# Kernel optimization log

Measured on AMD Instinct MI355X. Metric: run time of the kernel, lower is better.

Reference implementation:

```python
import jax, jax.numpy as jnp
import numpy as np


def setup_inputs() -> dict:
    key = jax.random.key(0)
    k1, k2, k3, k4, k5 = jax.random.split(key, 5)
    B, F, E, NF = 16384, 1024, 64, 32
    return {
        "input": jax.random.normal(k1, (B, F), dtype=jnp.float32),
        "fields": jax.random.randint(k2, (F,), 0, NF, dtype=jnp.int32),
        "w_weight": jax.random.normal(k3, (1, F), dtype=jnp.float32) * 0.02,
        "w_bias": jax.random.normal(k4, (1,), dtype=jnp.float32) * 0.02,
        "vs": jax.random.normal(k5, (NF, F, E), dtype=jnp.float32) * 0.05,
    }


def reference(input, fields, w_weight, w_bias, vs):
    # Linear (1st-order) term: [B, 1]
    linear = input @ w_weight.T + w_bias

    F = input.shape[1]
    # Gather field-aware embedding tables per feature: G[k, i, e] = vs[fields[k], i, e]
    G = vs[fields]  # [F, F, E]
    # A[i, j] = dot(vs[fields[j], i, :], vs[fields[i], j, :])
    A = jnp.einsum("jie,ije->ij", G, G)  # [F, F]
    # P[i, j] = sum_b input[b, i] * input[b, j]  (original sums over batch)
    P = input.T @ input  # [F, F]
    # second_order = sum_{i < j} A[i, j] * P[i, j]  (scalar, as in the source)
    second_order = jnp.sum(jnp.triu(A * P, k=1))

    return jax.nn.sigmoid(linear + second_order)
```

## Files before the change

### kernel.cpp

```cpp
#include <hip/hip_runtime.h>
#include <hip/hip_fp16.h>
#include <math.h>
#include <stdint.h>

#define FDIM 1024
#define BTOT 16384
#define EDIM 64
#define NFLD 32
#define NPANEL 4
#define NPAIRS 10

typedef _Float16 half8 __attribute__((ext_vector_type(8)));
typedef __fp16 fp16x2 __attribute__((ext_vector_type(2)));
typedef float f32x4 __attribute__((ext_vector_type(4)));

__device__ __forceinline__ uint32_t pk2(float a, float b){
  fp16x2 h = __builtin_amdgcn_cvt_pkrtz(a, b);
  return __builtin_bit_cast(uint32_t, h);
}

__device__ __forceinline__ void gload16(const void* g, void* l){
  __builtin_amdgcn_global_load_lds((const __attribute__((address_space(1))) void*)g,
                                   (__attribute__((address_space(3))) void*)l,
                                   16, 0, 0);
}

__device__ __forceinline__ float fget(const float4& v, int i){
  switch (i){ case 0: return v.x; case 1: return v.y; case 2: return v.z; default: return v.w; }
}

__device__ __forceinline__ int pairId(int ti, int tj){
  return ti * NPANEL - (ti * (ti + 1)) / 2 + tj;
}

__device__ __forceinline__ int CMAP(int col){
  return ((col & 3) << 6) | ((col >> 2) ^ ((col & 3) << 1));
}

__global__ __launch_bounds__(256) void transpose_kernel(
    const float* __restrict__ X, const float* __restrict__ w,
    uint4* __restrict__ Xbt, float* __restrict__ linp){
  const int t = threadIdx.x;
  const int bx = blockIdx.x;
  const int p  = bx & 3;
  const int kb = bx >> 2;
  const int ro = t >> 6;
  const int l  = t & 63;
  const int og = kb * 4 + ro;
  const int k0 = og * 8;
  const int c0 = p * 256;

  const float4 w4 = *(const float4*)(w + c0 + 4 * l);

  float4 rv[8];
#pragma unroll
  for (int r = 0; r < 8; ++r)
    rv[r] = *(const float4*)(X + (size_t)(k0 + r) * FDIM + c0 + 4 * l);

  uint4* dst = Xbt + ((size_t)p * 2048 + og) * 256;
#pragma unroll
  for (int i = 0; i < 4; ++i){
    uint4 ch;
    ch.x = pk2(fget(rv[0], i), fget(rv[1], i));
    ch.y = pk2(fget(rv[2], i), fget(rv[3], i));
    ch.z = pk2(fget(rv[4], i), fget(rv[5], i));
    ch.w = pk2(fget(rv[6], i), fget(rv[7], i));
    dst[(i << 6) | (l ^ (i << 1))] = ch;
  }

#pragma unroll
  for (int r = 0; r < 8; ++r){
    float lp = rv[r].x * w4.x + rv[r].y * w4.y + rv[r].z * w4.z + rv[r].w * w4.w;
#pragma unroll
    for (int off = 32; off; off >>= 1) lp += __shfl_xor(lp, off, 64);
    if (l == 0) linp[(size_t)p * BTOT + k0 + r] = lp;
  }
}

__global__ __launch_bounds__(256) void w2_kernel(
    const float* __restrict__ vs, const int* __restrict__ fields,
    _Float16* __restrict__ Wp){
  __shared__ float Si[32][68];
  __shared__ float Sj[32][68];
  __shared__ int gI[32], gJ[32];
  __shared__ int cnt[NFLD], pos[NFLD], off[NFLD + 1];
  __shared__ int permS[FDIM];
  const int t = threadIdx.x;

  if (t < NFLD) cnt[t] = 0;
  __syncthreads();
#pragma unroll
  for (int r = 0; r < 4; ++r) atomicAdd(&cnt[fields[t + 256 * r]], 1);
  __syncthreads();
  if (t == 0){
    int s = 0;
    for (int i = 0; i < NFLD; ++i){ off[i] = s; s += cnt[i]; }
    off[NFLD] = s;
  }
  __syncthreads();
  if (t < NFLD) pos[t] = off[t];
  __syncthreads();
#pragma unroll
  for (int r = 0; r < 4; ++r){
    const int idx = t + 256 * r;
    const int p = atomicAdd(&pos[fields[idx]], 1);
    permS[p] = idx;
  }
  __syncthreads();

  const int a = blockIdx.x >> 5, b = blockIdx.x & 31;
  const int oa = off[a], na = off[a + 1] - oa;
  const int ob = off[b], nb_ = off[b + 1] - ob;
  if (na == 0 || nb_ == 0) return;
  for (int ia0 = 0; ia0 < na; ia0 += 32){
    const int nac = min(32, na - ia0);
    for (int jb0 = 0; jb0 < nb_; jb0 += 32){
      const int nbc = min(32, nb_ - jb0);
      __syncthreads();
      if (t < 32){
        gI[t] = (t < nac) ? permS[oa + ia0 + t] : 0;
        gJ[t] = (t < nbc) ? permS[ob + jb0 + t] : 0;
      }
      __syncthreads();
#pragma unroll
      for (int rep = 0; rep < 2; ++rep){
        const int lidx = rep * 256 + t;
        const int r = lidx >> 4, e4 = (lidx & 15) * 4;
        if (r < nac)
          *(float4*)&Si[r][e4] = *(const float4*)(vs + ((size_t)b * FDIM + gI[r]) * EDIM + e4);
        if (r < nbc)
          *(float4*)&Sj[r][e4] = *(const float4*)(vs + ((size_t)a * FDIM + gJ[r]) * EDIM + e4);
      }
      __syncthreads();
      const int jr = t & 31;
      const int ir0 = t >> 5;
      for (int ko = 0; ko * 8 < nac; ++ko){
        const int ir = ko * 8 + ir0;
        if (ir < nac && jr < nbc){
          float dot = 0.f;
#pragma unroll
          for (int e4 = 0; e4 < EDIM; e4 += 4){
            const float4 x = *(const float4*)&Si[ir][e4];
            const float4 y = *(const float4*)&Sj[jr][e4];
            dot += x.x * y.x + x.y * y.y + x.z * y.z + x.w * y.w;
          }
          const int gi = gI[ir], gj = gJ[jr];
          const int pi = gi >> 8, pj = gj >> 8;
          if (pi <= pj){
            const float v = (gj > gi) ? dot : 0.f;
            const int li = gi & 255, lj = gj & 255;
            const int P  = pairId(pi, pj);
            const int w8 = (li >> 7) * 4 + (lj >> 6);
            const int mb = (li >> 4) & 7, r_ = li & 3;
            const int lane = ((li >> 2) & 3) * 16 + (lj & 15);
            const int nbv = (lj >> 4) & 3;
            const size_t o_ = (size_t)(P * 8 + w8) * 8192
                            + (size_t)((mb * 2 + (r_ >> 1)) * 64 + lane) * 8
                            + (r_ & 1) * 4 + nbv;
            Wp[o_] = (_Float16)v;
          }
        }
      }
    }
  }
}

__global__ __launch_bounds__(512, 1) void gram_kc(
    const uint4* __restrict__ Xbt, const _Float16* __restrict__ Wp,
    float* __restrict__ partial){
  __shared__ uint4 lds4[8192];
  const int t = threadIdx.x, w = t >> 6, lane = t & 63;
  const int orow = lane >> 4, rl = lane & 15;
  const int wr = w >> 2, wc = w & 3;
  const int b8 = blockIdx.x * 8;

#pragma unroll
  for (int p = 0; p < NPANEL; ++p)
#pragma unroll
    for (int q = 0; q < 4; ++q){
      const int m = q * 512 + t;
      const int o = m >> 8, c = m & 255;
      gload16(Xbt + ((size_t)p * 2048 + b8 + o) * 256 + c,
              lds4 + o * 1024 + p * 256 + c);
    }

  int swA[8], swB[4];
#pragma unroll
  for (int mb = 0; mb < 8; ++mb) swA[mb] = CMAP(wr * 128 + mb * 16 + rl);
#pragma unroll
  for (int nb = 0; nb < 4; ++nb) swB[nb] = CMAP(wc * 64 + nb * 16 + rl);

  float wsum = 0.f;

  auto loadB = [&](int tj, half8 (&bf)[2][4]){
#pragma unroll
    for (int s = 0; s < 2; ++s)
#pragma unroll
      for (int nb = 0; nb < 4; ++nb)
        bf[s][nb] = __builtin_bit_cast(half8,
            lds4[(s * 4 + orow) * 1024 + tj * 256 + swB[nb]]);
  };

  auto body = [&](int ti, int tj, const half8 (&bf)[2][4]){
    if (ti == tj && wr == 1 && wc < 2) return;

    const uint4* wp = (const uint4*)(Wp + (size_t)(pairId(ti, tj) * 8 + w) * 8192);
    half8 wreg[16];
#pragma unroll
    for (int q = 0; q < 16; ++q)
      wreg[q] = __builtin_bit_cast(half8, wp[q * 64 + lane]);

    f32x4 acc[8][4];
#pragma unroll
    for (int i = 0; i < 8; ++i)
#pragma unroll
      for (int j = 0; j < 4; ++j) acc[i][j] = {0.f, 0.f, 0.f, 0.f};
#pragma unroll
    for (int s = 0; s < 2; ++s)
#pragma unroll
      for (int mb = 0; mb < 8; ++mb){
        const half8 af = __builtin_bit_cast(half8,
            lds4[(s * 4 + orow) * 1024 + ti * 256 + swA[mb]]);
#pragma unroll
        for (int nb = 0; nb < 4; ++nb)
          acc[mb][nb] = __builtin_amdgcn_mfma_f32_16x16x32_f16(
              af, bf[s][nb], acc[mb][nb], 0, 0, 0);
      }
#pragma unroll
    for (int mb = 0; mb < 8; ++mb)
#pragma unroll
      for (int h = 0; h < 2; ++h){
        const half8 hv = wreg[mb * 2 + h];
#pragma unroll
        for (int r2 = 0; r2 < 2; ++r2)
#pragma unroll
          for (int nb = 0; nb < 4; ++nb)
            wsum += (float)hv[r2 * 4 + nb] * acc[mb][nb][2 * h + r2];
      }
  };

#define GRAM_GROUP(G, VM)                                         \
  asm volatile("s_waitcnt vmcnt(" #VM ")" ::: "memory");          \
  __builtin_amdgcn_s_barrier();                                   \
  {                                                               \
    half8 bf[2][4];                                               \
    loadB(G, bf);                                                 \
    _Pragma("unroll 1")                                           \
    for (int ti = 0; ti <= (G); ++ti) body(ti, (G), bf);          \
  }

  GRAM_GROUP(0, 12)
  GRAM_GROUP(1, 8)
  GRAM_GROUP(2, 4)
  GRAM_GROUP(3, 0)
#undef GRAM_GROUP

#pragma unroll
  for (int off = 32; off; off >>= 1) wsum += __shfl_xor(wsum, off, 64);
  __syncthreads();
  float* red = (float*)lds4;
  if (lane == 0) red[w] = wsum;
  __syncthreads();
  if (t == 0){
    float s = 0.f;
#pragma unroll
    for (int i = 0; i < 8; ++i) s += red[i];
    partial[blockIdx.x] = s;
  }
}

__global__ __launch_bounds__(256) void final_out(
    const float* __restrict__ partial, const float* __restrict__ linp,
    const float* __restrict__ wb, float* __restrict__ out){
  __shared__ float red[256];
  const int t = threadIdx.x;
  red[t] = partial[t];
  __syncthreads();
  for (int off = 128; off; off >>= 1){
    if (t < off) red[t] += red[t + off];
    __syncthreads();
  }
  const float stot = red[0] + wb[0];
  const int i = blockIdx.x * 256 + t;
  float z = stot;
#pragma unroll
  for (int p = 0; p < NPANEL; ++p) z += linp[(size_t)p * BTOT + i];
  out[i] = 1.f / (1.f + expf(-z));
}

extern "C" void kernel_launch(void* const* d_in, const int* in_sizes, int n_in,
                              void* d_out, int out_size, void* d_ws,
                              size_t ws_size, hipStream_t stream) {
  const float* X      = (const float*)d_in[0];
  const int* fields   = (const int*)d_in[1];
  const float* ww     = (const float*)d_in[2];
  const float* wbias  = (const float*)d_in[3];
  const float* vs     = (const float*)d_in[4];
  float* out          = (float*)d_out;

  char* ws = (char*)d_ws;
  float* partial = (float*)ws;
  float* linp = (float*)(ws + (64 << 10));
  _Float16* Wp = (_Float16*)(ws + (size_t)(4 << 20));
  uint4* Xbt = (uint4*)(ws + (size_t)(8 << 20));


  transpose_kernel<<<2048, 256, 0, stream>>>(X, ww, Xbt, linp);
  w2_kernel<<<NFLD * NFLD, 256, 0, stream>>>(vs, fields, Wp);
  gram_kc<<<256, 512, 0, stream>>>(Xbt, Wp, partial);
  final_out<<<BTOT / 256, 256, 0, stream>>>(partial, linp, wbias, out);
}
```

Measured before the change: 70.89 us.

## Fuse fp32-to-fp16 transpose and linear term into gram kernel

Removes the separate transpose kernel. The gram kernel now reads fp32 X directly, converts and packs it to fp16 in LDS, and computes the per-row linear term in registers. This saves a global round trip of the packed fp16 X and one kernel launch, and final_out now reads a single linear value per row. In exchange, the async global-to-LDS loads and the per-panel vmcnt pipelining are lost: all loads and conversion happen up front, followed by a block barrier.

```diff
diff --git a/kernel.cpp b/kernel.cpp
--- a/kernel.cpp
+++ b/kernel.cpp
@@ -19,12 +19,6 @@
   return __builtin_bit_cast(uint32_t, h);
 }
 
-__device__ __forceinline__ void gload16(const void* g, void* l){
-  __builtin_amdgcn_global_load_lds((const __attribute__((address_space(1))) void*)g,
-                                   (__attribute__((address_space(3))) void*)l,
-                                   16, 0, 0);
-}
-
 __device__ __forceinline__ float fget(const float4& v, int i){
   switch (i){ case 0: return v.x; case 1: return v.y; case 2: return v.z; default: return v.w; }
 }
@@ -35,46 +29,6 @@
 
 __device__ __forceinline__ int CMAP(int col){
   return ((col & 3) << 6) | ((col >> 2) ^ ((col & 3) << 1));
-}
-
-__global__ __launch_bounds__(256) void transpose_kernel(
-    const float* __restrict__ X, const float* __restrict__ w,
-    uint4* __restrict__ Xbt, float* __restrict__ linp){
-  const int t = threadIdx.x;
-  const int bx = blockIdx.x;
-  const int p  = bx & 3;
-  const int kb = bx >> 2;
-  const int ro = t >> 6;
-  const int l  = t & 63;
-  const int og = kb * 4 + ro;
-  const int k0 = og * 8;
-  const int c0 = p * 256;
-
-  const float4 w4 = *(const float4*)(w + c0 + 4 * l);
-
-  float4 rv[8];
-#pragma unroll
-  for (int r = 0; r < 8; ++r)
-    rv[r] = *(const float4*)(X + (size_t)(k0 + r) * FDIM + c0 + 4 * l);
-
-  uint4* dst = Xbt + ((size_t)p * 2048 + og) * 256;
-#pragma unroll
-  for (int i = 0; i < 4; ++i){
-    uint4 ch;
-    ch.x = pk2(fget(rv[0], i), fget(rv[1], i));
-    ch.y = pk2(fget(rv[2], i), fget(rv[3], i));
-    ch.z = pk2(fget(rv[4], i), fget(rv[5], i));
-    ch.w = pk2(fget(rv[6], i), fget(rv[7], i));
-    dst[(i << 6) | (l ^ (i << 1))] = ch;
-  }
-
-#pragma unroll
-  for (int r = 0; r < 8; ++r){
-    float lp = rv[r].x * w4.x + rv[r].y * w4.y + rv[r].z * w4.z + rv[r].w * w4.w;
-#pragma unroll
-    for (int off = 32; off; off >>= 1) lp += __shfl_xor(lp, off, 64);
-    if (l == 0) linp[(size_t)p * BTOT + k0 + r] = lp;
-  }
 }
 
 __global__ __launch_bounds__(256) void w2_kernel(
@@ -165,24 +119,53 @@
   }
 }
 
-__global__ __launch_bounds__(512, 1) void gram_kc(
-    const uint4* __restrict__ Xbt, const _Float16* __restrict__ Wp,
-    float* __restrict__ partial){
+__global__ __launch_bounds__(512, 1) void gram_fx(
+    const float* __restrict__ X, const float* __restrict__ w,
+    const _Float16* __restrict__ Wp,
+    float* __restrict__ partial, float* __restrict__ lin){
   __shared__ uint4 lds4[8192];
-  const int t = threadIdx.x, w = t >> 6, lane = t & 63;
+  const int t = threadIdx.x, wv = t >> 6, lane = t & 63;
   const int orow = lane >> 4, rl = lane & 15;
-  const int wr = w >> 2, wc = w & 3;
-  const int b8 = blockIdx.x * 8;
-
-#pragma unroll
-  for (int p = 0; p < NPANEL; ++p)
-#pragma unroll
-    for (int q = 0; q < 4; ++q){
-      const int m = q * 512 + t;
-      const int o = m >> 8, c = m & 255;
-      gload16(Xbt + ((size_t)p * 2048 + b8 + o) * 256 + c,
-              lds4 + o * 1024 + p * 256 + c);
+  const int wr = wv >> 2, wc = wv & 3;
+  const int k0 = blockIdx.x * 64 + wv * 8;
+
+  float lp[8];
+#pragma unroll
+  for (int r = 0; r < 8; ++r) lp[r] = 0.f;
+
+#pragma unroll 1
+  for (int p = 0; p < NPANEL; ++p){
+    const int c0 = p * 256;
+    float4 rv[8];
+#pragma unroll
+    for (int r = 0; r < 8; ++r)
+      rv[r] = *(const float4*)(X + (size_t)(k0 + r) * FDIM + c0 + 4 * lane);
+    const float4 w4 = *(const float4*)(w + c0 + 4 * lane);
+#pragma unroll
+    for (int r = 0; r < 8; ++r)
+      lp[r] += rv[r].x * w4.x + rv[r].y * w4.y + rv[r].z * w4.z + rv[r].w * w4.w;
+
+    uint4* base = lds4 + wv * 1024 + p * 256;
+#pragma unroll
+    for (int i = 0; i < 4; ++i){
+      uint4 ch;
+      ch.x = pk2(fget(rv[0], i), fget(rv[1], i));
+      ch.y = pk2(fget(rv[2], i), fget(rv[3], i));
+      ch.z = pk2(fget(rv[4], i), fget(rv[5], i));
+      ch.w = pk2(fget(rv[6], i), fget(rv[7], i));
+      base[(i << 6) | (lane ^ (i << 1))] = ch;
     }
+  }
+
+#pragma unroll
+  for (int r = 0; r < 8; ++r){
+    float v = lp[r];
+#pragma unroll
+    for (int off = 32; off; off >>= 1) v += __shfl_xor(v, off, 64);
+    if (lane == 0) lin[k0 + r] = v;
+  }
+
+  __syncthreads();
 
   int swA[8], swB[4];
 #pragma unroll
@@ -204,7 +187,7 @@
   auto body = [&](int ti, int tj, const half8 (&bf)[2][4]){
     if (ti == tj && wr == 1 && wc < 2) return;
 
-    const uint4* wp = (const uint4*)(Wp + (size_t)(pairId(ti, tj) * 8 + w) * 8192);
+    const uint4* wp = (const uint4*)(Wp + (size_t)(pairId(ti, tj) * 8 + wv) * 8192);
     half8 wreg[16];
 #pragma unroll
     for (int q = 0; q < 16; ++q)
@@ -239,27 +222,19 @@
       }
   };
 
-#define GRAM_GROUP(G, VM)                                         \
-  asm volatile("s_waitcnt vmcnt(" #VM ")" ::: "memory");          \
-  __builtin_amdgcn_s_barrier();                                   \
-  {                                                               \
-    half8 bf[2][4];                                               \
-    loadB(G, bf);                                                 \
-    _Pragma("unroll 1")                                           \
-    for (int ti = 0; ti <= (G); ++ti) body(ti, (G), bf);          \
-  }
-
-  GRAM_GROUP(0, 12)
-  GRAM_GROUP(1, 8)
-  GRAM_GROUP(2, 4)
-  GRAM_GROUP(3, 0)
-#undef GRAM_GROUP
+#pragma unroll 1
+  for (int G = 0; G < NPANEL; ++G){
+    half8 bf[2][4];
+    loadB(G, bf);
+#pragma unroll 1
+    for (int ti = 0; ti <= G; ++ti) body(ti, G, bf);
+  }
 
 #pragma unroll
   for (int off = 32; off; off >>= 1) wsum += __shfl_xor(wsum, off, 64);
   __syncthreads();
   float* red = (float*)lds4;
-  if (lane == 0) red[w] = wsum;
+  if (lane == 0) red[wv] = wsum;
   __syncthreads();
   if (t == 0){
     float s = 0.f;
@@ -270,7 +245,7 @@
 }
 
 __global__ __launch_bounds__(256) void final_out(
-    const float* __restrict__ partial, const float* __restrict__ linp,
+    const float* __restrict__ partial, const float* __restrict__ lin,
     const float* __restrict__ wb, float* __restrict__ out){
   __shared__ float red[256];
   const int t = threadIdx.x;
@@ -282,9 +257,7 @@
   }
   const float stot = red[0] + wb[0];
   const int i = blockIdx.x * 256 + t;
-  float z = stot;
-#pragma unroll
-  for (int p = 0; p < NPANEL; ++p) z += linp[(size_t)p * BTOT + i];
+  const float z = lin[i] + stot;
   out[i] = 1.f / (1.f + expf(-z));
 }
 
@@ -300,13 +273,11 @@
 
   char* ws = (char*)d_ws;
   float* partial = (float*)ws;
-  float* linp = (float*)(ws + (64 << 10));
+  float* lin = (float*)(ws + (64 << 10));
   _Float16* Wp = (_Float16*)(ws + (size_t)(4 << 20));
-  uint4* Xbt = (uint4*)(ws + (size_t)(8 << 20));
-
-
-  transpose_kernel<<<2048, 256, 0, stream>>>(X, ww, Xbt, linp);
+
+
   w2_kernel<<<NFLD * NFLD, 256, 0, stream>>>(vs, fields, Wp);
-  gram_kc<<<256, 512, 0, stream>>>(Xbt, Wp, partial);
-  final_out<<<BTOT / 256, 256, 0, stream>>>(partial, linp, wbias, out);
-}
+  gram_fx<<<256, 512, 0, stream>>>(X, ww, Wp, partial, lin);
+  final_out<<<BTOT / 256, 256, 0, stream>>>(partial, lin, wbias, out);
+}
```

Measured after the change: 61.17 us (median of 2 runs). 1.16x faster.
